# Kernel optimization log

Hardware: AMD Instinct MI355X
Metric: run time of the kernel (lower is better)

The kernel has to match this reference:

```python
import jax, jax.numpy as jnp
import numpy as np

# tokenizer constants (MoonBoard-like 11x18 grid)
X_COORD_START = 10
Y_COORD_START = 21
EOS_TOKEN = 39
MAX_REACH = 5.0
WINDOW_SIZE = 4
PENALTY_SCALE = 1.0


def setup_inputs() -> dict:
    key = jax.random.key(0)
    input_ids = jax.random.randint(key, (2048, 2048), 0, EOS_TOKEN, dtype=jnp.int32)
    return {"input_ids": input_ids}


def _compact_coords(input_ids):
    """Extract (x, y) hold tokens, compact valid holds to the front per row."""
    x_tok = input_ids[:, 2::2]
    y_tok = input_ids[:, 3::2]
    H = min(x_tok.shape[1], y_tok.shape[1])
    x_tok, y_tok = x_tok[:, :H], y_tok[:, :H]
    valid = ((x_tok >= X_COORD_START) & (x_tok < Y_COORD_START)
             & (y_tok >= Y_COORD_START) & (y_tok < EOS_TOKEN))
    # stable argsort moves valid entries to the front, preserving order
    order = jnp.argsort(jnp.logical_not(valid), axis=1)  # stable by default
    xv = jnp.take_along_axis(x_tok, order, axis=1)
    yv = jnp.take_along_axis(y_tok, order, axis=1)
    count = valid.sum(axis=1)  # [B] number of valid holds per sequence
    x_c = (xv - X_COORD_START).astype(jnp.float32)
    y_c = (yv - Y_COORD_START + 1).astype(jnp.float32)
    return x_c, y_c, count


def _loss(x_c, y_c, count):
    B, H = x_c.shape
    W = WINDOW_SIZE
    if H < W + 1:
        return jnp.float32(0.0)
    min_d = None
    for j in range(1, W + 1):  # small fixed window loop
        dx = x_c[:, W:] - x_c[:, W - j:H - j]  # hold i vs hold i-j, [B, H-W]
        dy = y_c[:, W:] - y_c[:, W - j:H - j]
        sq = dx * dx + dy * dy
        d = jnp.where(sq > 0, jnp.sqrt(jnp.where(sq > 0, sq, 1.0)), 0.0)
        min_d = d if min_d is None else jnp.minimum(min_d, d)
    viol = jnp.maximum(min_d - MAX_REACH, 0.0)  # [B, H-W]
    i_idx = jnp.arange(W, H)
    check_mask = (i_idx[None, :] < count[:, None]).astype(viol.dtype)
    seq_pen = jnp.sum(viol * check_mask, axis=1)  # [B]
    num_checks = jnp.maximum(count - W, 1).astype(viol.dtype)
    seq_valid = count >= W + 1
    per_seq = jnp.where(seq_valid, seq_pen / num_checks, 0.0)
    nvs = seq_valid.sum().astype(viol.dtype)
    total = per_seq.sum()
    return jnp.where(nvs > 0, PENALTY_SCALE * total / nvs, jnp.float32(0.0))


def reference(input_ids):
    x_c, y_c, count = _compact_coords(input_ids)
    return _loss(x_c, y_c, count)
```

## Files before the change

kernel.cpp:

```cpp
#include <hip/hip_runtime.h>

#define X_COORD_START 10
#define Y_COORD_START 21
#define EOS_TOKEN     39
#define MAX_REACH     5.0f
#define W             4

#define ROW_LEN 2048
#define NROWS   2048
#define ROWS_PER_BLOCK 8
#define BLOCK_A (ROWS_PER_BLOCK * 64)
#define NBLOCKS_A (NROWS / ROWS_PER_BLOCK)
#define BUFCAP  512

__device__ __forceinline__ int is_valid(int x, int y) {
    return ((unsigned)(x - X_COORD_START) < (unsigned)(Y_COORD_START - X_COORD_START)) &
           ((unsigned)(y - Y_COORD_START) < (unsigned)(EOS_TOKEN - Y_COORD_START));
}

__device__ __forceinline__ int pack_xy(int x, int y) {
    return (x - X_COORD_START) | ((y - (Y_COORD_START - 1)) << 8);
}

__global__ __launch_bounds__(BLOCK_A)
void reach_rows_kernel(const int* __restrict__ ids, float2* __restrict__ part) {
    const int t    = threadIdx.x;
    const int lane = t & 63;
    const int wid  = t >> 6;
    const int row  = blockIdx.x * ROWS_PER_BLOCK + wid;

    __shared__ int lbuf[ROWS_PER_BLOCK][BUFCAP];
    int* rowbuf = lbuf[wid];

    const int* base = ids + (size_t)row * ROW_LEN;

    int4 v[8];
    #pragma unroll
    for (int c = 0; c < 8; ++c)
        v[c] = *reinterpret_cast<const int4*>(base + 4 * (c * 64 + lane));

    const unsigned long long below = (1ull << lane) - 1ull;
    int off = 0;
    #pragma unroll
    for (int c = 0; c < 8; ++c) {
        const int j  = c * 64 + lane;
        const int va = (j > 0) & is_valid(v[c].x, v[c].y);
        const int vb = is_valid(v[c].z, v[c].w);
        const unsigned long long ma = __ballot(va);
        const unsigned long long mb = __ballot(vb);
        const int pa = __popcll(ma & below);
        const int pb = __popcll(mb & below);
        if (va) rowbuf[off + pa + pb]      = pack_xy(v[c].x, v[c].y);
        if (vb) rowbuf[off + pa + pb + va] = pack_xy(v[c].z, v[c].w);
        off += __popcll(ma) + __popcll(mb);
    }
    const int count = off;

    float acc = 0.f;
    for (int i = W + lane; i < count; i += 64) {
        const int pi = rowbuf[i];
        const int xi = pi & 0xff, yi = pi >> 8;
        int mn = 0x7fffffff;
        #pragma unroll
        for (int jj = 1; jj <= W; ++jj) {
            const int pj = rowbuf[i - jj];
            const int dx = xi - (pj & 0xff);
            const int dy = yi - (pj >> 8);
            mn = min(mn, dx * dx + dy * dy);
        }
        const float d = (mn > 0) ? sqrtf((float)mn) : 0.f;
        acc += fmaxf(d - MAX_REACH, 0.f);
    }

    #pragma unroll
    for (int o = 32; o > 0; o >>= 1) acc += __shfl_down(acc, o);
    if (lane == 0) {
        const int sv = count >= W + 1;
        part[row] = make_float2(sv ? acc / (float)max(count - W, 1) : 0.f,
                                sv ? 1.f : 0.f);
    }
}

__global__ __launch_bounds__(512)
void reach_final_kernel(const float2* __restrict__ part, float* __restrict__ out) {
    const int t    = threadIdx.x;
    const int lane = t & 63;
    const int wid  = t >> 6;

    __shared__ float ss[8], sn[8];

    const float4* p4 = reinterpret_cast<const float4*>(part);
    const float4 a = p4[t];
    const float4 b = p4[t + 512];
    float s = a.x + a.z + b.x + b.z;
    float n = a.y + a.w + b.y + b.w;

    #pragma unroll
    for (int o = 32; o > 0; o >>= 1) {
        s += __shfl_down(s, o);
        n += __shfl_down(n, o);
    }
    if (lane == 0) { ss[wid] = s; sn[wid] = n; }
    __syncthreads();
    if (t == 0) {
        float st = 0.f, nt = 0.f;
        #pragma unroll
        for (int w = 0; w < 8; ++w) { st += ss[w]; nt += sn[w]; }
        out[0] = (nt > 0.f) ? st / nt : 0.f;
    }
}

extern "C" void kernel_launch(void* const* d_in, const int* in_sizes, int n_in,
                              void* d_out, int out_size, void* d_ws, size_t ws_size,
                              hipStream_t stream) {
    const int* ids = (const int*)d_in[0];
    float*     out = (float*)d_out;
    float2*    part = (float2*)d_ws;

    reach_rows_kernel<<<NBLOCKS_A, BLOCK_A, 0, stream>>>(ids, part);
    reach_final_kernel<<<1, 512, 0, stream>>>(part, out);
}
```

Baseline: 11.06 us.

## Split each row across two waves and pre-reduce partials per block

Each row is now processed by two wavefronts that each load and compact half of the row. Wave counts are exchanged through shared memory so the second wave writes at the right offset, and both waves split the distance loop. Per-block partials are reduced in-kernel, which shrinks the final kernel to a single wave. This aims to raise memory-level parallelism and shorten the per-wave serial chain, at the cost of extra block-wide barriers.

```diff
diff --git a/kernel.cpp b/kernel.cpp
--- a/kernel.cpp
+++ b/kernel.cpp
@@ -8,8 +8,9 @@
 
 #define ROW_LEN 2048
 #define NROWS   2048
-#define ROWS_PER_BLOCK 8
-#define BLOCK_A (ROWS_PER_BLOCK * 64)
+#define ROWS_PER_BLOCK 4
+#define WAVES_PER_ROW  2
+#define BLOCK_A (ROWS_PER_BLOCK * WAVES_PER_ROW * 64)
 #define NBLOCKS_A (NROWS / ROWS_PER_BLOCK)
 #define BUFCAP  512
 
@@ -26,38 +27,55 @@
 void reach_rows_kernel(const int* __restrict__ ids, float2* __restrict__ part) {
     const int t    = threadIdx.x;
     const int lane = t & 63;
-    const int wid  = t >> 6;
-    const int row  = blockIdx.x * ROWS_PER_BLOCK + wid;
+    const int wave = t >> 6;
+    const int r    = wave >> 1;
+    const int sub  = wave & 1;
+    const int row  = blockIdx.x * ROWS_PER_BLOCK + r;
 
-    __shared__ int lbuf[ROWS_PER_BLOCK][BUFCAP];
-    int* rowbuf = lbuf[wid];
+    __shared__ int   lbuf[ROWS_PER_BLOCK][BUFCAP];
+    __shared__ int   wcnt[ROWS_PER_BLOCK][WAVES_PER_ROW];
+    __shared__ float racc[ROWS_PER_BLOCK][WAVES_PER_ROW];
+    int* rowbuf = lbuf[r];
 
     const int* base = ids + (size_t)row * ROW_LEN;
 
-    int4 v[8];
+    int4 v[4];
     #pragma unroll
-    for (int c = 0; c < 8; ++c)
-        v[c] = *reinterpret_cast<const int4*>(base + 4 * (c * 64 + lane));
+    for (int c = 0; c < 4; ++c)
+        v[c] = *reinterpret_cast<const int4*>(base + 4 * ((sub * 4 + c) * 64 + lane));
 
     const unsigned long long below = (1ull << lane) - 1ull;
+    int itemA[4], itemB[4], locA[4];
+    int vA[4], vB[4];
     int off = 0;
     #pragma unroll
-    for (int c = 0; c < 8; ++c) {
-        const int j  = c * 64 + lane;
+    for (int c = 0; c < 4; ++c) {
+        const int j  = (sub * 4 + c) * 64 + lane;
         const int va = (j > 0) & is_valid(v[c].x, v[c].y);
         const int vb = is_valid(v[c].z, v[c].w);
         const unsigned long long ma = __ballot(va);
         const unsigned long long mb = __ballot(vb);
-        const int pa = __popcll(ma & below);
-        const int pb = __popcll(mb & below);
-        if (va) rowbuf[off + pa + pb]      = pack_xy(v[c].x, v[c].y);
-        if (vb) rowbuf[off + pa + pb + va] = pack_xy(v[c].z, v[c].w);
+        locA[c]  = off + __popcll(ma & below) + __popcll(mb & below);
+        itemA[c] = pack_xy(v[c].x, v[c].y);
+        itemB[c] = pack_xy(v[c].z, v[c].w);
+        vA[c] = va; vB[c] = vb;
         off += __popcll(ma) + __popcll(mb);
     }
-    const int count = off;
+    if (lane == 0) wcnt[r][sub] = off;
+    __syncthreads();
+
+    const int wbase = sub ? wcnt[r][0] : 0;
+    const int count = wcnt[r][0] + wcnt[r][1];
+
+    #pragma unroll
+    for (int c = 0; c < 4; ++c) {
+        if (vA[c]) rowbuf[wbase + locA[c]]         = itemA[c];
+        if (vB[c]) rowbuf[wbase + locA[c] + vA[c]] = itemB[c];
+    }
+    __syncthreads();
 
     float acc = 0.f;
-    for (int i = W + lane; i < count; i += 64) {
+    for (int i = W + sub * 64 + lane; i < count; i += 128) {
         const int pi = rowbuf[i];
         const int xi = pi & 0xff, yi = pi >> 8;
         int mn = 0x7fffffff;
@@ -74,49 +92,50 @@
 
     #pragma unroll
     for (int o = 32; o > 0; o >>= 1) acc += __shfl_down(acc, o);
-    if (lane == 0) {
-        const int sv = count >= W + 1;
-        part[row] = make_float2(sv ? acc / (float)max(count - W, 1) : 0.f,
-                                sv ? 1.f : 0.f);
+    if (lane == 0) racc[r][sub] = acc;
+    __syncthreads();
+
+    if (t == 0) {
+        float bs = 0.f, bn = 0.f;
+        #pragma unroll
+        for (int rr = 0; rr < ROWS_PER_BLOCK; ++rr) {
+            const int   c  = wcnt[rr][0] + wcnt[rr][1];
+            const float s  = racc[rr][0] + racc[rr][1];
+            const int   sv = c >= W + 1;
+            bs += sv ? s / (float)max(c - W, 1) : 0.f;
+            bn += sv ? 1.f : 0.f;
+        }
+        part[blockIdx.x] = make_float2(bs, bn);
     }
 }
 
-__global__ __launch_bounds__(512)
+__global__ __launch_bounds__(64)
 void reach_final_kernel(const float2* __restrict__ part, float* __restrict__ out) {
-    const int t    = threadIdx.x;
-    const int lane = t & 63;
-    const int wid  = t >> 6;
+    const int lane = threadIdx.x;
+    const float4* p4 = reinterpret_cast<const float4*>(part);
 
-    __shared__ float ss[8], sn[8];
-
-    const float4* p4 = reinterpret_cast<const float4*>(part);
-    const float4 a = p4[t];
-    const float4 b = p4[t + 512];
-    float s = a.x + a.z + b.x + b.z;
-    float n = a.y + a.w + b.y + b.w;
-
+    float s = 0.f, n = 0.f;
+    #pragma unroll
+    for (int c = 0; c < 4; ++c) {
+        const float4 a = p4[c * 64 + lane];
+        s += a.x + a.z;
+        n += a.y + a.w;
+    }
     #pragma unroll
     for (int o = 32; o > 0; o >>= 1) {
         s += __shfl_down(s, o);
         n += __shfl_down(n, o);
     }
-    if (lane == 0) { ss[wid] = s; sn[wid] = n; }
-    __syncthreads();
-    if (t == 0) {
-        float st = 0.f, nt = 0.f;
-        #pragma unroll
-        for (int w = 0; w < 8; ++w) { st += ss[w]; nt += sn[w]; }
-        out[0] = (nt > 0.f) ? st / nt : 0.f;
-    }
+    if (lane == 0) out[0] = (n > 0.f) ? s / n : 0.f;
 }
 
 extern "C" void kernel_launch(void* const* d_in, const int* in_sizes, int n_in,
                               void* d_out, int out_size, void* d_ws, size_t ws_size,
                               hipStream_t stream) {
-    const int* ids = (const int*)d_in[0];
-    float*     out = (float*)d_out;
+    const int* ids  = (const int*)d_in[0];
+    float*     out  = (float*)d_out;
     float2*    part = (float2*)d_ws;
 
     reach_rows_kernel<<<NBLOCKS_A, BLOCK_A, 0, stream>>>(ids, part);
-    reach_final_kernel<<<1, 512, 0, stream>>>(part, out);
+    reach_final_kernel<<<1, 64, 0, stream>>>(part, out);
 }
```

After: 11.25 us. No clear change (+1.7%).

## Fuse row and final reduction kernels via cooperative grid sync

Applied to the files above, without the earlier changes.

Merges the per-row penalty kernel and the final reduction kernel into one cooperative launch. Each block first pre-reduces its rows in shared memory, then a grid-wide sync lets block 0 reduce the 256 per-block partials. This removes a second kernel launch and its dependency gap, but adds a grid barrier and the overhead of a cooperative launch, which can cost more than a plain launch.

```diff
diff --git a/kernel.cpp b/kernel.cpp
--- a/kernel.cpp
+++ b/kernel.cpp
@@ -1,4 +1,7 @@
 #include <hip/hip_runtime.h>
+#include <hip/hip_cooperative_groups.h>
+
+namespace cg = cooperative_groups;
 
 #define X_COORD_START 10
 #define Y_COORD_START 21
@@ -9,8 +12,8 @@
 #define ROW_LEN 2048
 #define NROWS   2048
 #define ROWS_PER_BLOCK 8
-#define BLOCK_A (ROWS_PER_BLOCK * 64)
-#define NBLOCKS_A (NROWS / ROWS_PER_BLOCK)
+#define BLOCK   (ROWS_PER_BLOCK * 64)
+#define NBLOCKS (NROWS / ROWS_PER_BLOCK)
 #define BUFCAP  512
 
 __device__ __forceinline__ int is_valid(int x, int y) {
@@ -22,14 +25,17 @@
     return (x - X_COORD_START) | ((y - (Y_COORD_START - 1)) << 8);
 }
 
-__global__ __launch_bounds__(BLOCK_A)
-void reach_rows_kernel(const int* __restrict__ ids, float2* __restrict__ part) {
+__global__ __launch_bounds__(BLOCK)
+void reach_fused_kernel(const int* __restrict__ ids,
+                        float2* __restrict__ part,
+                        float* __restrict__ out) {
     const int t    = threadIdx.x;
     const int lane = t & 63;
     const int wid  = t >> 6;
     const int row  = blockIdx.x * ROWS_PER_BLOCK + wid;
 
-    __shared__ int lbuf[ROWS_PER_BLOCK][BUFCAP];
+    __shared__ int    lbuf[ROWS_PER_BLOCK][BUFCAP];
+    __shared__ float2 rpart[ROWS_PER_BLOCK];
     int* rowbuf = lbuf[wid];
 
     const int* base = ids + (size_t)row * ROW_LEN;
@@ -76,47 +82,43 @@
     for (int o = 32; o > 0; o >>= 1) acc += __shfl_down(acc, o);
     if (lane == 0) {
         const int sv = count >= W + 1;
-        part[row] = make_float2(sv ? acc / (float)max(count - W, 1) : 0.f,
-                                sv ? 1.f : 0.f);
+        rpart[wid] = make_float2(sv ? acc / (float)max(count - W, 1) : 0.f,
+                                 sv ? 1.f : 0.f);
     }
-}
+    __syncthreads();
 
-__global__ __launch_bounds__(512)
-void reach_final_kernel(const float2* __restrict__ part, float* __restrict__ out) {
-    const int t    = threadIdx.x;
-    const int lane = t & 63;
-    const int wid  = t >> 6;
+    if (t == 0) {
+        float bs = 0.f, bn = 0.f;
+        #pragma unroll
+        for (int rr = 0; rr < ROWS_PER_BLOCK; ++rr) { bs += rpart[rr].x; bn += rpart[rr].y; }
+        part[blockIdx.x] = make_float2(bs, bn);
+    }
 
-    __shared__ float ss[8], sn[8];
+    cg::this_grid().sync();
 
-    const float4* p4 = reinterpret_cast<const float4*>(part);
-    const float4 a = p4[t];
-    const float4 b = p4[t + 512];
-    float s = a.x + a.z + b.x + b.z;
-    float n = a.y + a.w + b.y + b.w;
-
-    #pragma unroll
-    for (int o = 32; o > 0; o >>= 1) {
-        s += __shfl_down(s, o);
-        n += __shfl_down(n, o);
-    }
-    if (lane == 0) { ss[wid] = s; sn[wid] = n; }
-    __syncthreads();
-    if (t == 0) {
-        float st = 0.f, nt = 0.f;
+    if (blockIdx.x == 0 && wid == 0) {
+        const float4* p4 = reinterpret_cast<const float4*>(part);
+        const float4 a = p4[lane];
+        const float4 b = p4[lane + 64];
+        float s = a.x + a.z + b.x + b.z;
+        float n = a.y + a.w + b.y + b.w;
         #pragma unroll
-        for (int w = 0; w < 8; ++w) { st += ss[w]; nt += sn[w]; }
-        out[0] = (nt > 0.f) ? st / nt : 0.f;
+        for (int o = 32; o > 0; o >>= 1) {
+            s += __shfl_down(s, o);
+            n += __shfl_down(n, o);
+        }
+        if (lane == 0) out[0] = (n > 0.f) ? s / n : 0.f;
     }
 }
 
 extern "C" void kernel_launch(void* const* d_in, const int* in_sizes, int n_in,
                               void* d_out, int out_size, void* d_ws, size_t ws_size,
                               hipStream_t stream) {
-    const int* ids = (const int*)d_in[0];
-    float*     out = (float*)d_out;
+    const int* ids  = (const int*)d_in[0];
+    float*     out  = (float*)d_out;
     float2*    part = (float2*)d_ws;
 
-    reach_rows_kernel<<<NBLOCKS_A, BLOCK_A, 0, stream>>>(ids, part);
-    reach_final_kernel<<<1, 512, 0, stream>>>(part, out);
+    void* args[] = { (void*)&ids, (void*)&part, (void*)&out };
+    hipLaunchCooperativeKernel((const void*)reach_fused_kernel,
+                               dim3(NBLOCKS), dim3(BLOCK), args, 0, stream);
 }
```

Measured after the change: 43.54 us. 3.94x slower.
